# Kernel optimization log

Measured on AMD Instinct MI355X. Metric: run time of the kernel, lower is better.

The kernel has to match this reference:

```python
import jax, jax.numpy as jnp
import numpy as np

TOKENS = 4096      # batch*seq flattened
D_IN = 4096        # in_features
D_OUT = 16384      # out_features (4*d_model FFN)


def setup_inputs() -> dict:
    key = jax.random.key(0)
    k1, k2, k3, k4 = jax.random.split(key, 4)
    x = jax.random.normal(k1, (TOKENS, D_IN), dtype=jnp.float32)
    # int8 quantized weight in [-127, 127]
    quantized_weight = jax.random.randint(k2, (D_OUT, D_IN), -127, 128, dtype=jnp.int8)
    # per-output-row scale, positive and small (abs-max / 127 style)
    weight_scale = jax.random.uniform(k3, (D_OUT, 1), dtype=jnp.float32, minval=1e-4, maxval=0.02)
    bias = jax.random.normal(k4, (D_OUT,), dtype=jnp.float32)
    return {"x": x, "quantized_weight": quantized_weight,
            "weight_scale": weight_scale, "bias": bias}


def reference(x, quantized_weight, weight_scale, bias):
    # Dequantize: int8 -> x.dtype, then per-row scale (materializes full weight,
    # exactly as the torch module does).
    w = quantized_weight.astype(x.dtype) * weight_scale  # [D_OUT, D_IN]
    # F.linear: x @ w.T + bias
    return jnp.dot(x, w.T) + bias
```

## Files before the change

### kernel.cpp

```cpp
#include <hip/hip_runtime.h>

#define TOKENS 4096
#define DIN    4096
#define DOUT   16384

#define BM 128
#define BN 128
#define BK 32

#define X_BYTES ((size_t)TOKENS * DIN * 2)
#define W_BYTES ((size_t)DOUT   * DIN * 2)

typedef __attribute__((ext_vector_type(8))) short short8;
typedef __attribute__((ext_vector_type(4))) float f32x4;

__device__ __forceinline__ unsigned short f2bf(float f) {
    unsigned u = __builtin_bit_cast(unsigned, f);
    u += 0x7fffu + ((u >> 16) & 1u);
    return (unsigned short)(u >> 16);
}

#define GLOAD_LDS16(gptr, lptr)                                                        \
    __builtin_amdgcn_global_load_lds(                                                  \
        (const __attribute__((address_space(1))) unsigned int*)(gptr),                 \
        (__attribute__((address_space(3))) unsigned int*)(lptr), 16, 0, 0)

__global__ __launch_bounds__(256)
void cvt_x_kernel(const float* __restrict__ in, unsigned short* __restrict__ out) {
    const size_t base = ((size_t)blockIdx.x * 256 + threadIdx.x) * 8;
    const float4 a = *(const float4*)&in[base];
    const float4 b = *(const float4*)&in[base + 4];
    uint4 o;
    o.x = (unsigned)f2bf(a.x) | ((unsigned)f2bf(a.y) << 16);
    o.y = (unsigned)f2bf(a.z) | ((unsigned)f2bf(a.w) << 16);
    o.z = (unsigned)f2bf(b.x) | ((unsigned)f2bf(b.y) << 16);
    o.w = (unsigned)f2bf(b.z) | ((unsigned)f2bf(b.w) << 16);
    *(uint4*)&out[base] = o;
}

__global__ __launch_bounds__(256)
void cvt_w_kernel(const int* __restrict__ in, unsigned short* __restrict__ out) {
    const size_t base = ((size_t)blockIdx.x * 256 + threadIdx.x) * 8;
    const int4 a = *(const int4*)&in[base];
    const int4 b = *(const int4*)&in[base + 4];
    uint4 o;
    o.x = (unsigned)f2bf((float)a.x) | ((unsigned)f2bf((float)a.y) << 16);
    o.y = (unsigned)f2bf((float)a.z) | ((unsigned)f2bf((float)a.w) << 16);
    o.z = (unsigned)f2bf((float)b.x) | ((unsigned)f2bf((float)b.y) << 16);
    o.w = (unsigned)f2bf((float)b.z) | ((unsigned)f2bf((float)b.w) << 16);
    *(uint4*)&out[base] = o;
}

__global__ __launch_bounds__(256, 2)
void gemm_bf16_kernel(const unsigned short* __restrict__ xa,
                      const unsigned short* __restrict__ wb,
                      const float* __restrict__ scale,
                      const float* __restrict__ bias,
                      float* __restrict__ out) {
    __shared__ unsigned short As[BM * BK];
    __shared__ unsigned short Bs[BN * BK];

    const int tid  = threadIdx.x;
    const int lane = tid & 63;
    const int wave = tid >> 6;
    const int wm   = wave >> 1;
    const int wn   = wave & 1;
    const int quad = lane >> 4;
    const int l16  = lane & 15;

    const int m0 = blockIdx.x * BM;
    const int n0 = blockIdx.y * BN;

    size_t ga[2], gb[2];
    #pragma unroll
    for (int i = 0; i < 2; ++i) {
        const int p    = i * 256 + tid;
        const int row  = p >> 2;
        const int gq   = (p & 3) ^ ((row >> 1) & 3);
        ga[i] = (size_t)(m0 + row) * DIN + gq * 8;
        gb[i] = (size_t)(n0 + row) * DIN + gq * 8;
    }
    unsigned short* lA[2];
    unsigned short* lB[2];
    #pragma unroll
    for (int i = 0; i < 2; ++i) {
        const int chunk0 = i * 256 + wave * 64;
        lA[i] = &As[chunk0 * 8];
        lB[i] = &Bs[chunk0 * 8];
    }

    int aoff[4], boff[4];
    #pragma unroll
    for (int i = 0; i < 4; ++i) {
        const int rowA = wm * 64 + i * 16 + l16;
        aoff[i] = (rowA * 4 + (quad ^ ((rowA >> 1) & 3))) * 8;
        const int rowB = wn * 64 + i * 16 + l16;
        boff[i] = (rowB * 4 + (quad ^ ((rowB >> 1) & 3))) * 8;
    }

    f32x4 acc[4][4];
    #pragma unroll
    for (int i = 0; i < 4; ++i)
        #pragma unroll
        for (int j = 0; j < 4; ++j)
            acc[i][j] = (f32x4){0.f, 0.f, 0.f, 0.f};

    for (int k0 = 0; k0 < DIN; k0 += BK) {
        __syncthreads();
        GLOAD_LDS16(xa + ga[0] + k0, lA[0]);
        GLOAD_LDS16(xa + ga[1] + k0, lA[1]);
        GLOAD_LDS16(wb + gb[0] + k0, lB[0]);
        GLOAD_LDS16(wb + gb[1] + k0, lB[1]);
        __syncthreads();

        short8 af[4], bfv[4];
        #pragma unroll
        for (int i = 0; i < 4; ++i) af[i]  = *(const short8*)&As[aoff[i]];
        #pragma unroll
        for (int j = 0; j < 4; ++j) bfv[j] = *(const short8*)&Bs[boff[j]];

        #pragma unroll
        for (int i = 0; i < 4; ++i)
            #pragma unroll
            for (int j = 0; j < 4; ++j)
                acc[i][j] = __builtin_amdgcn_mfma_f32_16x16x32_bf16(af[i], bfv[j], acc[i][j], 0, 0, 0);
    }

    #pragma unroll
    for (int j = 0; j < 4; ++j) {
        const int col = n0 + wn * 64 + j * 16 + l16;
        const float s = scale[col];
        const float b = bias[col];
        #pragma unroll
        for (int i = 0; i < 4; ++i) {
            const int row0 = m0 + wm * 64 + i * 16 + quad * 4;
            #pragma unroll
            for (int r = 0; r < 4; ++r)
                out[(size_t)(row0 + r) * DOUT + col] = acc[i][j][r] * s + b;
        }
    }
}

#define LDSS 40
__global__ __launch_bounds__(256, 2)
void gemm_fallback_kernel(const float* __restrict__ x, const int* __restrict__ qw,
                          const float* __restrict__ scale, const float* __restrict__ bias,
                          float* __restrict__ out) {
    __shared__ unsigned short As[BM * LDSS];
    __shared__ unsigned short Bs[BN * LDSS];
    const int tid = threadIdx.x, lane = tid & 63, wave = tid >> 6;
    const int wm = wave >> 1, wn = wave & 1, quad = lane >> 4, l16 = lane & 15;
    const int m0 = blockIdx.x * BM, n0 = blockIdx.y * BN;
    const int srow = tid >> 3, scol = (tid & 7) * 4;
    f32x4 acc[4][4];
    #pragma unroll
    for (int i = 0; i < 4; ++i)
        #pragma unroll
        for (int j = 0; j < 4; ++j) acc[i][j] = (f32x4){0.f, 0.f, 0.f, 0.f};
    for (int k0 = 0; k0 < DIN; k0 += BK) {
        __syncthreads();
        #pragma unroll
        for (int p = 0; p < 4; ++p) {
            const int r = p * 32 + srow;
            const float4 v = *(const float4*)&x[(size_t)(m0 + r) * DIN + k0 + scol];
            const unsigned a01 = (unsigned)f2bf(v.x) | ((unsigned)f2bf(v.y) << 16);
            const unsigned a23 = (unsigned)f2bf(v.z) | ((unsigned)f2bf(v.w) << 16);
            *(unsigned long long*)&As[r * LDSS + scol] =
                (unsigned long long)a01 | ((unsigned long long)a23 << 32);
        }
        #pragma unroll
        for (int p = 0; p < 4; ++p) {
            const int r = p * 32 + srow;
            const int4 v = *(const int4*)&qw[(size_t)(n0 + r) * DIN + k0 + scol];
            const unsigned b01 = (unsigned)f2bf((float)v.x) | ((unsigned)f2bf((float)v.y) << 16);
            const unsigned b23 = (unsigned)f2bf((float)v.z) | ((unsigned)f2bf((float)v.w) << 16);
            *(unsigned long long*)&Bs[r * LDSS + scol] =
                (unsigned long long)b01 | ((unsigned long long)b23 << 32);
        }
        __syncthreads();
        short8 af[4], bfv[4];
        #pragma unroll
        for (int i = 0; i < 4; ++i)
            af[i] = *(const short8*)&As[(wm * 64 + i * 16 + l16) * LDSS + quad * 8];
        #pragma unroll
        for (int j = 0; j < 4; ++j)
            bfv[j] = *(const short8*)&Bs[(wn * 64 + j * 16 + l16) * LDSS + quad * 8];
        #pragma unroll
        for (int i = 0; i < 4; ++i)
            #pragma unroll
            for (int j = 0; j < 4; ++j)
                acc[i][j] = __builtin_amdgcn_mfma_f32_16x16x32_bf16(af[i], bfv[j], acc[i][j], 0, 0, 0);
    }
    #pragma unroll
    for (int j = 0; j < 4; ++j) {
        const int col = n0 + wn * 64 + j * 16 + l16;
        const float s = scale[col], b = bias[col];
        #pragma unroll
        for (int i = 0; i < 4; ++i) {
            const int row0 = m0 + wm * 64 + i * 16 + quad * 4;
            #pragma unroll
            for (int r = 0; r < 4; ++r)
                out[(size_t)(row0 + r) * DOUT + col] = acc[i][j][r] * s + b;
        }
    }
}

extern "C" void kernel_launch(void* const* d_in, const int* in_sizes, int n_in,
                              void* d_out, int out_size, void* d_ws, size_t ws_size,
                              hipStream_t stream) {
    const float* x     = (const float*)d_in[0];
    const int*   qw    = (const int*)d_in[1];
    const float* scale = (const float*)d_in[2];
    const float* bias  = (const float*)d_in[3];
    float*       out   = (float*)d_out;

    if (ws_size >= X_BYTES + W_BYTES) {
        unsigned short* x_bf = (unsigned short*)d_ws;
        unsigned short* w_bf = (unsigned short*)((char*)d_ws + X_BYTES);
        cvt_x_kernel<<<dim3((TOKENS * DIN) / (256 * 8)), dim3(256), 0, stream>>>(x, x_bf);
        cvt_w_kernel<<<dim3((DOUT * DIN) / (256 * 8)), dim3(256), 0, stream>>>(qw, w_bf);
        gemm_bf16_kernel<<<dim3(TOKENS / BM, DOUT / BN), dim3(256), 0, stream>>>(
            x_bf, w_bf, scale, bias, out);
    } else {
        gemm_fallback_kernel<<<dim3(TOKENS / BM, DOUT / BN), dim3(256), 0, stream>>>(
            x, qw, scale, bias, out);
    }
}
```

Measured before the change: 1.087 ms.

## Rewrite bf16 GEMM as 256x256x64 double-buffered pipelined kernel with XCD-aware tile mapping

```diff
diff --git a/kernel.cpp b/kernel.cpp
--- a/kernel.cpp
+++ b/kernel.cpp
@@ -4,9 +4,10 @@
 #define DIN    4096
 #define DOUT   16384
 
-#define BM 128
-#define BN 128
-#define BK 32
+#define BM 256
+#define BN 256
+#define BK 64
+#define NT (DIN / BK)
 
 #define X_BYTES ((size_t)TOKENS * DIN * 2)
 #define W_BYTES ((size_t)DOUT   * DIN * 2)
@@ -51,115 +52,188 @@
     *(uint4*)&out[base] = o;
 }
 
-__global__ __launch_bounds__(256, 2)
+__global__ __launch_bounds__(512, 2)
 void gemm_bf16_kernel(const unsigned short* __restrict__ xa,
                       const unsigned short* __restrict__ wb,
                       const float* __restrict__ scale,
                       const float* __restrict__ bias,
                       float* __restrict__ out) {
-    __shared__ unsigned short As[BM * BK];
-    __shared__ unsigned short Bs[BN * BK];
+    __shared__ unsigned short smem[2 * 32768];
 
     const int tid  = threadIdx.x;
     const int lane = tid & 63;
     const int wave = tid >> 6;
-    const int wm   = wave >> 1;
-    const int wn   = wave & 1;
+    const int wm   = wave >> 2;
+    const int wn   = wave & 3;
     const int quad = lane >> 4;
     const int l16  = lane & 15;
 
-    const int m0 = blockIdx.x * BM;
-    const int n0 = blockIdx.y * BN;
-
-    size_t ga[2], gb[2];
-    #pragma unroll
+    const int nwg = (TOKENS / BM) * (DOUT / BN);
+    const int wg  = ((int)blockIdx.x & 7) * (nwg >> 3) + ((int)blockIdx.x >> 3);
+    const int m0  = (wg & 15) * BM;
+    const int n0  = (wg >> 4) * BN;
+
+    int gAo[2], gBo[2];
+#pragma unroll
     for (int i = 0; i < 2; ++i) {
-        const int p    = i * 256 + tid;
-        const int row  = p >> 2;
-        const int gq   = (p & 3) ^ ((row >> 1) & 3);
-        ga[i] = (size_t)(m0 + row) * DIN + gq * 8;
-        gb[i] = (size_t)(n0 + row) * DIN + gq * 8;
-    }
-    unsigned short* lA[2];
-    unsigned short* lB[2];
-    #pragma unroll
-    for (int i = 0; i < 2; ++i) {
-        const int chunk0 = i * 256 + wave * 64;
-        lA[i] = &As[chunk0 * 8];
-        lB[i] = &Bs[chunk0 * 8];
-    }
-
-    int aoff[4], boff[4];
-    #pragma unroll
-    for (int i = 0; i < 4; ++i) {
-        const int rowA = wm * 64 + i * 16 + l16;
-        aoff[i] = (rowA * 4 + (quad ^ ((rowA >> 1) & 3))) * 8;
-        const int rowB = wn * 64 + i * 16 + l16;
-        boff[i] = (rowB * 4 + (quad ^ ((rowB >> 1) & 3))) * 8;
-    }
-
-    f32x4 acc[4][4];
-    #pragma unroll
-    for (int i = 0; i < 4; ++i)
-        #pragma unroll
+        const int c  = i * 512 + tid;
+        const int r  = c >> 3;
+        const int gc = (c & 7) ^ (r & 7);
+        gAo[i] = (m0 + r) * DIN + gc * 8;
+        gBo[i] = (n0 + r) * DIN + gc * 8;
+    }
+
+#define STAGE(b, isA, h, kt)                                                             \
+    do {                                                                                 \
+        const unsigned short* _s = (isA) ? xa : wb;                                      \
+        const int _g0 = ((isA) ? gAo[0] : gBo[0]) + (h) * 128 * DIN + (kt) * BK;         \
+        const int _g1 = ((isA) ? gAo[1] : gBo[1]) + (h) * 128 * DIN + (kt) * BK;         \
+        unsigned short* _d =                                                             \
+            &smem[(b) * 32768 + ((isA) ? 0 : 16384) + ((h) * 1024 + wave * 64) * 8];     \
+        GLOAD_LDS16(_s + _g0, _d);                                                       \
+        GLOAD_LDS16(_s + _g1, _d + 4096);                                                \
+    } while (0)
+
+    const int s7    = l16 & 7;
+    const int cx0   = (quad ^ s7) * 8;
+    const int cx1   = ((quad ^ s7) ^ 4) * 8;
+    const int aoff0 = (wm * 128 + l16) * 64 + cx0;
+    const int aoff1 = (wm * 128 + l16) * 64 + cx1;
+    const int boff0 = (wn * 64 + l16) * 64 + cx0;
+    const int boff1 = (wn * 64 + l16) * 64 + cx1;
+
+#define READ_A(mh)                                                                       \
+    do {                                                                                 \
+        _Pragma("unroll") for (int i = 0; i < 4; ++i) {                                  \
+            af[i * 2]     = *(const short8*)&pA[aoff0 + (mh) * 4096 + i * 1024];         \
+            af[i * 2 + 1] = *(const short8*)&pA[aoff1 + (mh) * 4096 + i * 1024];         \
+        }                                                                                \
+    } while (0)
+
+#define READ_B(dst, nh)                                                                  \
+    do {                                                                                 \
+        _Pragma("unroll") for (int j = 0; j < 2; ++j) {                                  \
+            dst[j * 2]     = *(const short8*)&pB[boff0 + (nh) * 2048 + j * 1024];        \
+            dst[j * 2 + 1] = *(const short8*)&pB[boff1 + (nh) * 2048 + j * 1024];        \
+        }                                                                                \
+    } while (0)
+
+#define MFMA_Q(mh, nh, bv)                                                               \
+    do {                                                                                 \
+        __builtin_amdgcn_s_setprio(1);                                                   \
+        _Pragma("unroll") for (int i = 0; i < 4; ++i)                                    \
+            _Pragma("unroll") for (int j = 0; j < 2; ++j) {                              \
+                acc[(mh) * 4 + i][(nh) * 2 + j] = __builtin_amdgcn_mfma_f32_16x16x32_bf16( \
+                    af[i * 2], bv[j * 2], acc[(mh) * 4 + i][(nh) * 2 + j], 0, 0, 0);     \
+                acc[(mh) * 4 + i][(nh) * 2 + j] = __builtin_amdgcn_mfma_f32_16x16x32_bf16( \
+                    af[i * 2 + 1], bv[j * 2 + 1], acc[(mh) * 4 + i][(nh) * 2 + j], 0, 0, 0); \
+            }                                                                            \
+        __builtin_amdgcn_s_setprio(0);                                                   \
+    } while (0)
+
+    STAGE(0, 1, 0, 0);
+    STAGE(0, 0, 0, 0);
+    STAGE(0, 0, 1, 0);
+    STAGE(0, 1, 1, 0);
+    STAGE(1, 0, 0, 1);
+    STAGE(1, 0, 1, 1);
+    STAGE(1, 1, 0, 1);
+
+    f32x4 acc[8][4];
+#pragma unroll
+    for (int i = 0; i < 8; ++i)
+#pragma unroll
         for (int j = 0; j < 4; ++j)
             acc[i][j] = (f32x4){0.f, 0.f, 0.f, 0.f};
 
-    for (int k0 = 0; k0 < DIN; k0 += BK) {
-        __syncthreads();
-        GLOAD_LDS16(xa + ga[0] + k0, lA[0]);
-        GLOAD_LDS16(xa + ga[1] + k0, lA[1]);
-        GLOAD_LDS16(wb + gb[0] + k0, lB[0]);
-        GLOAD_LDS16(wb + gb[1] + k0, lB[1]);
-        __syncthreads();
-
-        short8 af[4], bfv[4];
-        #pragma unroll
-        for (int i = 0; i < 4; ++i) af[i]  = *(const short8*)&As[aoff[i]];
-        #pragma unroll
-        for (int j = 0; j < 4; ++j) bfv[j] = *(const short8*)&Bs[boff[j]];
-
-        #pragma unroll
-        for (int i = 0; i < 4; ++i)
-            #pragma unroll
-            for (int j = 0; j < 4; ++j)
-                acc[i][j] = __builtin_amdgcn_mfma_f32_16x16x32_bf16(af[i], bfv[j], acc[i][j], 0, 0, 0);
-    }
-
-    #pragma unroll
-    for (int j = 0; j < 4; ++j) {
-        const int col = n0 + wn * 64 + j * 16 + l16;
+    asm volatile("s_waitcnt vmcnt(6)" ::: "memory");
+    __builtin_amdgcn_s_barrier();
+
+#pragma unroll 2
+    for (int t = 0; t < NT; ++t) {
+        const int cur = t & 1;
+        const unsigned short* pA = &smem[cur * 32768];
+        const unsigned short* pB = pA + 16384;
+        short8 af[8], bq0[4], bq1[4];
+
+        READ_A(0);
+        READ_B(bq0, 0);
+        if (t + 1 < NT) STAGE(cur ^ 1, 1, 1, t + 1);
+        __builtin_amdgcn_s_barrier();
+        asm volatile("s_waitcnt lgkmcnt(0)" ::: "memory");
+        MFMA_Q(0, 0, bq0);
+        __builtin_amdgcn_s_barrier();
+
+        READ_B(bq1, 1);
+        __builtin_amdgcn_s_barrier();
+        asm volatile("s_waitcnt lgkmcnt(0)" ::: "memory");
+        MFMA_Q(0, 1, bq1);
+        __builtin_amdgcn_s_barrier();
+
+        READ_A(1);
+        if (t + 2 < NT) {
+            STAGE(cur, 0, 0, t + 2);
+            STAGE(cur, 0, 1, t + 2);
+        }
+        __builtin_amdgcn_s_barrier();
+        asm volatile("s_waitcnt lgkmcnt(0)" ::: "memory");
+        MFMA_Q(1, 1, bq1);
+        __builtin_amdgcn_s_barrier();
+
+        if (t + 2 < NT) STAGE(cur, 1, 0, t + 2);
+        __builtin_amdgcn_s_barrier();
+        asm volatile("s_waitcnt lgkmcnt(0)" ::: "memory");
+        MFMA_Q(1, 0, bq0);
+        if (t < NT - 2) {
+            asm volatile("s_waitcnt vmcnt(6)" ::: "memory");
+        } else if (t == NT - 2) {
+            asm volatile("s_waitcnt vmcnt(0)" ::: "memory");
+        }
+        __builtin_amdgcn_s_barrier();
+    }
+
+#undef STAGE
+#undef READ_A
+#undef READ_B
+#undef MFMA_Q
+
+#pragma unroll
+    for (int aj = 0; aj < 4; ++aj) {
+        const int col = n0 + wn * 64 + aj * 16 + l16;
         const float s = scale[col];
         const float b = bias[col];
-        #pragma unroll
-        for (int i = 0; i < 4; ++i) {
-            const int row0 = m0 + wm * 64 + i * 16 + quad * 4;
-            #pragma unroll
+#pragma unroll
+        for (int ai = 0; ai < 8; ++ai) {
+            const int row0 = m0 + wm * 128 + ai * 16 + quad * 4;
+#pragma unroll
             for (int r = 0; r < 4; ++r)
-                out[(size_t)(row0 + r) * DOUT + col] = acc[i][j][r] * s + b;
-        }
-    }
-}
-
+                out[(size_t)(row0 + r) * DOUT + col] = acc[ai][aj][r] * s + b;
+        }
+    }
+}
+
+#define FBM 128
+#define FBN 128
+#define FBK 32
 #define LDSS 40
 __global__ __launch_bounds__(256, 2)
 void gemm_fallback_kernel(const float* __restrict__ x, const int* __restrict__ qw,
                           const float* __restrict__ scale, const float* __restrict__ bias,
                           float* __restrict__ out) {
-    __shared__ unsigned short As[BM * LDSS];
-    __shared__ unsigned short Bs[BN * LDSS];
+    __shared__ unsigned short As[FBM * LDSS];
+    __shared__ unsigned short Bs[FBN * LDSS];
     const int tid = threadIdx.x, lane = tid & 63, wave = tid >> 6;
     const int wm = wave >> 1, wn = wave & 1, quad = lane >> 4, l16 = lane & 15;
-    const int m0 = blockIdx.x * BM, n0 = blockIdx.y * BN;
+    const int m0 = blockIdx.x * FBM, n0 = blockIdx.y * FBN;
     const int srow = tid >> 3, scol = (tid & 7) * 4;
     f32x4 acc[4][4];
-    #pragma unroll
+#pragma unroll
     for (int i = 0; i < 4; ++i)
-        #pragma unroll
+#pragma unroll
         for (int j = 0; j < 4; ++j) acc[i][j] = (f32x4){0.f, 0.f, 0.f, 0.f};
-    for (int k0 = 0; k0 < DIN; k0 += BK) {
+    for (int k0 = 0; k0 < DIN; k0 += FBK) {
         __syncthreads();
-        #pragma unroll
+#pragma unroll
         for (int p = 0; p < 4; ++p) {
             const int r = p * 32 + srow;
             const float4 v = *(const float4*)&x[(size_t)(m0 + r) * DIN + k0 + scol];
@@ -168,7 +242,7 @@
             *(unsigned long long*)&As[r * LDSS + scol] =
                 (unsigned long long)a01 | ((unsigned long long)a23 << 32);
         }
-        #pragma unroll
+#pragma unroll
         for (int p = 0; p < 4; ++p) {
             const int r = p * 32 + srow;
             const int4 v = *(const int4*)&qw[(size_t)(n0 + r) * DIN + k0 + scol];
@@ -179,26 +253,26 @@
         }
         __syncthreads();
         short8 af[4], bfv[4];
-        #pragma unroll
+#pragma unroll
         for (int i = 0; i < 4; ++i)
             af[i] = *(const short8*)&As[(wm * 64 + i * 16 + l16) * LDSS + quad * 8];
-        #pragma unroll
+#pragma unroll
         for (int j = 0; j < 4; ++j)
             bfv[j] = *(const short8*)&Bs[(wn * 64 + j * 16 + l16) * LDSS + quad * 8];
-        #pragma unroll
+#pragma unroll
         for (int i = 0; i < 4; ++i)
-            #pragma unroll
+#pragma unroll
             for (int j = 0; j < 4; ++j)
                 acc[i][j] = __builtin_amdgcn_mfma_f32_16x16x32_bf16(af[i], bfv[j], acc[i][j], 0, 0, 0);
     }
-    #pragma unroll
+#pragma unroll
     for (int j = 0; j < 4; ++j) {
         const int col = n0 + wn * 64 + j * 16 + l16;
         const float s = scale[col], b = bias[col];
-        #pragma unroll
+#pragma unroll
         for (int i = 0; i < 4; ++i) {
             const int row0 = m0 + wm * 64 + i * 16 + quad * 4;
-            #pragma unroll
+#pragma unroll
             for (int r = 0; r < 4; ++r)
                 out[(size_t)(row0 + r) * DOUT + col] = acc[i][j][r] * s + b;
         }
@@ -219,10 +293,10 @@
         unsigned short* w_bf = (unsigned short*)((char*)d_ws + X_BYTES);
         cvt_x_kernel<<<dim3((TOKENS * DIN) / (256 * 8)), dim3(256), 0, stream>>>(x, x_bf);
         cvt_w_kernel<<<dim3((DOUT * DIN) / (256 * 8)), dim3(256), 0, stream>>>(qw, w_bf);
-        gemm_bf16_kernel<<<dim3(TOKENS / BM, DOUT / BN), dim3(256), 0, stream>>>(
+        gemm_bf16_kernel<<<dim3((TOKENS / BM) * (DOUT / BN)), dim3(512), 0, stream>>>(
             x_bf, w_bf, scale, bias, out);
     } else {
-        gemm_fallback_kernel<<<dim3(TOKENS / BM, DOUT / BN), dim3(256), 0, stream>>>(
+        gemm_fallback_kernel<<<dim3(TOKENS / FBM, DOUT / FBN), dim3(256), 0, stream>>>(
             x, qw, scale, bias, out);
     }
 }
```

New measurement: 990.0 us. 1.1x faster.
